# Kernel optimization log

Hardware: AMD Instinct MI355X
Metric: run time of the kernel (lower is better)

## Reference

```python
import jax, jax.numpy as jnp
import numpy as np

N_NODES, N_EDGES, HID = 30000, 480000, 128
N_GRAPHS, N_CLASSES = 128, 6
BN_EPS, ADD_SCORE = 1e-5, 0.5


def setup_inputs():
    key = jax.random.key(0)
    ks = jax.random.split(key, 12)
    g = lambda i, shape: jax.random.normal(ks[i], shape, jnp.float32) * 0.05
    return dict(
        x=jax.random.normal(ks[0], (N_NODES, HID), jnp.float32),
        edge_index=jax.random.randint(ks[1], (2, N_EDGES), 0, N_NODES, jnp.int32),
        batch=jnp.sort(jax.random.randint(ks[2], (N_NODES,), 0, N_GRAPHS, jnp.int32)),
        Wl=g(3, (6, HID, HID)), bl=jnp.zeros((6, HID), jnp.float32),
        Wr=g(4, (6, HID, HID)),
        gamma=jnp.ones((6, HID), jnp.float32), beta=jnp.zeros((6, HID), jnp.float32),
        Wlin=g(5, (3, HID, 2 * HID)), blin=jnp.zeros((3, HID), jnp.float32),
        Wp=g(6, (3, 2 * HID)), bp=jnp.zeros((3,), jnp.float32),
        Wf1=g(7, (HID, HID)), bf1=jnp.zeros((HID,), jnp.float32),
        Wf2=g(8, (N_CLASSES, HID)), bf2=jnp.zeros((N_CLASSES,), jnp.float32),
    )


def _sage(x, src, dst, emf, Wl_i, bl_i, Wr_i, N):
    # PyG SAGEConv: lin_l(mean_{j->i} x_j) + lin_r(x_i); emf masks dead edges
    msg = x[src] * emf[:, None]                              # [E,H]
    s = jax.ops.segment_sum(msg, dst, num_segments=N)
    c = jax.ops.segment_sum(emf, dst, num_segments=N)
    mean = s / jnp.maximum(c, 1.0)[:, None]
    return mean @ Wl_i.T + bl_i + x @ Wr_i.T


def _bn(x, g, b, nvf):
    # training-mode BatchNorm over valid (non-merged-away) nodes only
    cnt = jnp.maximum(nvf.sum(), 1.0)
    mu = (x * nvf[:, None]).sum(0) / cnt
    var = (((x - mu) ** 2) * nvf[:, None]).sum(0) / cnt
    return g * (x - mu) * jax.lax.rsqrt(var + BN_EPS) + b


def _edge_pool(x, src, dst, emb, nvb, Wp_i, bp_i, N, E):
    h = x.shape[1]
    # raw edge score = Linear(cat(x[src], x[dst]))
    raw = (x @ Wp_i[:h])[src] + (x @ Wp_i[h:])[dst] + bp_i   # [E]
    neg = jnp.finfo(x.dtype).min
    mx = jax.ops.segment_max(jnp.where(emb, raw, neg), dst, num_segments=N)
    z = jnp.where(emb, jnp.exp(jnp.where(emb, raw - mx[dst], 0.0)), 0.0)
    den = jax.ops.segment_sum(z, dst, num_segments=N)
    score = z / jnp.maximum(den, 1e-16)[dst] + ADD_SCORE     # softmax per dst + 0.5

    # greedy edge matching in descending score order (sequential, int-only carry)
    order = jnp.argsort(-jnp.where(emb, jax.lax.stop_gradient(score), -jnp.inf))

    def step(carry, i):
        matched, cluster, chosen = carry
        s, t = src[i], dst[i]
        ok = emb[i] & (~matched[s]) & (~matched[t]) & (s != t)
        rep, oth = jnp.minimum(s, t), jnp.maximum(s, t)
        matched = matched.at[s].set(matched[s] | ok)
        matched = matched.at[t].set(matched[t] | ok)
        cluster = cluster.at[oth].set(jnp.where(ok, rep, cluster[oth]))
        chosen = chosen.at[rep].set(jnp.where(ok, i, chosen[rep]))
        return (matched, cluster, chosen), None

    init = (~nvb, jnp.arange(N, dtype=jnp.int32), jnp.full((N,), -1, jnp.int32))
    (matched, cluster, chosen), _ = jax.lax.scan(step, init, order)

    # merged node = (x_s + x_t) * score(chosen edge); singleton score = 1
    nscore = jnp.where(chosen >= 0, score[jnp.maximum(chosen, 0)], 1.0)
    new_x = jax.ops.segment_sum(x, cluster, num_segments=N) * nscore[:, None]
    nvb2 = nvb & (cluster == jnp.arange(N, dtype=jnp.int32))
    # remap edges to cluster representatives; coalesce duplicates (self-loops kept, as PyG)
    key = jnp.where(emb, cluster[src] * N + cluster[dst], -1)  # N*N < 2**31
    uk = jnp.unique(key, size=E, fill_value=-1)
    emb2 = uk >= 0
    ukc = jnp.maximum(uk, 0)
    return new_x, ukc // N, ukc % N, emb2, nvb2


def reference(x, edge_index, batch, Wl, bl, Wr, gamma, beta, Wlin, blin, Wp, bp, Wf1, bf1, Wf2, bf2):
    N, E = x.shape[0], edge_index.shape[1]
    src, dst = edge_index[0], edge_index[1]
    emb = jnp.ones((E,), bool)   # edge-valid mask (fixed-shape graph coarsening)
    nvb = jnp.ones((N,), bool)   # node-valid mask
    for blk in range(3):
        emf, nvf = emb.astype(x.dtype), nvb.astype(x.dtype)
        i = 2 * blk
        h = _bn(jax.nn.relu(_sage(x, src, dst, emf, Wl[i], bl[i], Wr[i], N)), gamma[i], beta[i], nvf)
        h2 = _bn(jax.nn.relu(_sage(h, src, dst, emf, Wl[i + 1], bl[i + 1], Wr[i + 1], N)), gamma[i + 1], beta[i + 1], nvf)
        x = jnp.concatenate([h2, h], axis=1) @ Wlin[blk].T + blin[blk]  # dropout = identity (eval)
        x, src, dst, emb, nvb = _edge_pool(x, src, dst, emb, nvb, Wp[blk], bp[blk], N, E)
    nvf = nvb.astype(x.dtype)
    sums = jax.ops.segment_sum(x * nvf[:, None], batch, num_segments=N_GRAPHS)
    cnt = jax.ops.segment_sum(nvf, batch, num_segments=N_GRAPHS)
    pooled = sums / jnp.maximum(cnt, 1.0)[:, None]           # global_mean_pool
    hfc = jax.nn.relu(pooled @ Wf1.T + bf1)
    return jax.nn.log_softmax(hfc @ Wf2.T + bf2, axis=1)
```

## Files before the change

### kernel.cpp

```cpp
#include <hip/hip_runtime.h>
#include <stdint.h>

#define NN 30000
#define NE 480000
#define HID 128
#define NG 128
#define NC 6
#define BN_EPS 1e-5f
#define WPB 938

typedef unsigned int u32;
typedef unsigned long long u64;

__global__ void k_init(const int* __restrict__ ei, int* srcA, int* dstA, int* nvb,
                       int* scal, int* b3, int* i2, float* gbuf) {
  int t = blockIdx.x * 256 + threadIdx.x;
  if (t < NE) { srcA[t] = ei[t]; dstA[t] = ei[NE + t]; }
  if (t < NN) nvb[t] = 1;
  if (t < 2 * NN) { b3[t] = 0; i2[t] = 0; }
  if (t < NG * HID + NG) gbuf[t] = 0.f;
  if (t == 0) { scal[0] = NE; scal[1] = 0; }
}

__global__ void k_csr_count(const int* __restrict__ pE, const int* __restrict__ src,
                            const int* __restrict__ dst, int* __restrict__ cnt,
                            int* __restrict__ icnt, const int* __restrict__ nvb,
                            int* __restrict__ pcnt) {
  int t = blockIdx.x * 256 + threadIdx.x;
  if (t < NN && nvb[t]) atomicAdd(pcnt, 1);
  if (t < *pE) {
    int s = src[t], d = dst[t];
    atomicAdd(&cnt[d], 1);
    if (s != d) { atomicAdd(&icnt[s], 1); atomicAdd(&icnt[d], 1); }
  }
}

__global__ __launch_bounds__(1024) void k_scan2(const int* __restrict__ in0, int* __restrict__ out0,
                                                const int* __restrict__ in1, int* __restrict__ out1) {
  const int* in = blockIdx.x ? in1 : in0;
  int* out = blockIdx.x ? out1 : out0;
  __shared__ int part[1024];
  int t = threadIdx.x;
  int chunk = (NN + 1023) / 1024;
  int b = t * chunk, e = b + chunk;
  if (b > NN) b = NN;
  if (e > NN) e = NN;
  int s = 0;
  for (int i = b; i < e; i++) s += in[i];
  part[t] = s;
  __syncthreads();
  for (int off = 1; off < 1024; off <<= 1) {
    int v = (t >= off) ? part[t - off] : 0;
    __syncthreads();
    part[t] += v;
    __syncthreads();
  }
  int excl = (t == 0) ? 0 : part[t - 1];
  for (int i = b; i < e; i++) { out[i] = excl; excl += in[i]; }
  if (t == 0) out[NN] = part[1023];
}

__global__ void k_csr_scatter(const int* __restrict__ pE, const int* __restrict__ src,
                              const int* __restrict__ dst, const int* __restrict__ coff,
                              int* __restrict__ cursor, int* __restrict__ eids,
                              const int* __restrict__ ioff, int* __restrict__ icur,
                              int* __restrict__ ieids) {
  int e = blockIdx.x * 256 + threadIdx.x;
  if (e >= *pE) return;
  int s = src[e], d = dst[e];
  int pos = coff[d] + atomicAdd(&cursor[d], 1);
  eids[pos] = e;
  if (s != d) {
    int p1 = ioff[s] + atomicAdd(&icur[s], 1); ieids[p1] = e;
    int p2 = ioff[d] + atomicAdd(&icur[d], 1); ieids[p2] = e;
  }
}

__global__ __launch_bounds__(256) void k_sage_gather(
    const int* __restrict__ coff, const int* __restrict__ eids,
    const int* __restrict__ src, const float* __restrict__ x,
    float* __restrict__ mean) {
  int grp = threadIdx.x >> 5;
  int lane = threadIdx.x & 31;
  int n = blockIdx.x * 8 + grp;
  if (n >= NN) return;
  int b = coff[n], e2 = coff[n + 1];
  float4 acc = make_float4(0.f, 0.f, 0.f, 0.f);
  for (int i = b; i < e2; i++) {
    int s = src[eids[i]];
    float4 v = *(const float4*)(x + (size_t)s * HID + lane * 4);
    acc.x += v.x; acc.y += v.y; acc.z += v.z; acc.w += v.w;
  }
  float inv = 1.0f / fmaxf((float)(e2 - b), 1.0f);
  acc.x *= inv; acc.y *= inv; acc.z *= inv; acc.w *= inv;
  *(float4*)(mean + (size_t)n * HID + lane * 4) = acc;
}

__global__ __launch_bounds__(256) void gemm_dual(
    const float* __restrict__ A1, const float* __restrict__ W1,
    const float* __restrict__ A2, const float* __restrict__ W2,
    const float* __restrict__ bias, float* __restrict__ out,
    int M, int ldw, int relu, double* __restrict__ bnsum) {
  if (blockIdx.x == 0 && threadIdx.x < 2 * HID) bnsum[threadIdx.x] = 0.0;
  __shared__ float As[64][33];
  __shared__ float Ws[32][132];
  int row0 = blockIdx.x * 64;
  int tid = threadIdx.x;
  int cid = tid & 31;
  int rid = tid >> 5;
  float acc[8][4];
#pragma unroll
  for (int r = 0; r < 8; r++)
#pragma unroll
    for (int c = 0; c < 4; c++) acc[r][c] = 0.f;

  for (int srcI = 0; srcI < 2; ++srcI) {
    const float* A = srcI ? A2 : A1;
    const float* W = srcI ? W2 : W1;
    for (int kc = 0; kc < 128; kc += 32) {
#pragma unroll
      for (int i = 0; i < 2; ++i) {
        int idx = tid + i * 256;
        int r = idx >> 3;
        int c4 = (idx & 7) << 2;
        int gr = row0 + r;
        float4 v = make_float4(0.f, 0.f, 0.f, 0.f);
        if (gr < M) v = *(const float4*)(A + (size_t)gr * 128 + kc + c4);
        As[r][c4 + 0] = v.x; As[r][c4 + 1] = v.y; As[r][c4 + 2] = v.z; As[r][c4 + 3] = v.w;
      }
#pragma unroll
      for (int i = 0; i < 4; ++i) {
        int idx = tid + i * 256;
        int j = idx >> 3;
        int c4 = (idx & 7) << 2;
        float4 v = *(const float4*)(W + (size_t)j * ldw + kc + c4);
        Ws[c4 + 0][j] = v.x; Ws[c4 + 1][j] = v.y; Ws[c4 + 2][j] = v.z; Ws[c4 + 3][j] = v.w;
      }
      __syncthreads();
#pragma unroll
      for (int kk = 0; kk < 32; ++kk) {
        float4 w = *(const float4*)(&Ws[kk][cid * 4]);
#pragma unroll
        for (int r = 0; r < 8; ++r) {
          float a = As[rid * 8 + r][kk];
          acc[r][0] += a * w.x; acc[r][1] += a * w.y; acc[r][2] += a * w.z; acc[r][3] += a * w.w;
        }
      }
      __syncthreads();
    }
  }
#pragma unroll
  for (int r = 0; r < 8; ++r) {
    int gr = row0 + rid * 8 + r;
    if (gr >= M) continue;
#pragma unroll
    for (int c = 0; c < 4; ++c) {
      float v = acc[r][c] + bias[cid * 4 + c];
      if (relu) v = fmaxf(v, 0.f);
      out[(size_t)gr * 128 + cid * 4 + c] = v;
    }
  }
}

__global__ __launch_bounds__(128) void k_bn_stats(const float* __restrict__ x,
                                                  const int* __restrict__ nvb,
                                                  double* __restrict__ sums) {
  int k = threadIdx.x;
  int n0 = blockIdx.x * 64;
  float s = 0.f, q = 0.f;
  for (int r = 0; r < 64; r++) {
    int n = n0 + r;
    if (n >= NN) break;
    if (!nvb[n]) continue;
    float v = x[(size_t)n * HID + k];
    s += v; q += v * v;
  }
  atomicAdd(&sums[k], (double)s);
  atomicAdd(&sums[HID + k], (double)q);
}

__global__ void k_bn_apply(float* __restrict__ x, const double* __restrict__ sums,
                           const int* __restrict__ cnt, const float* __restrict__ gamma,
                           const float* __restrict__ beta) {
  int t = blockIdx.x * 256 + threadIdx.x;
  if (t >= NN * HID) return;
  int k = t & 127;
  double c = (double)((*cnt > 1) ? *cnt : 1);
  double mu = sums[k] / c;
  double var = sums[HID + k] / c - mu * mu;
  if (var < 0.0) var = 0.0;
  float inv = (float)(1.0 / sqrt(var + (double)BN_EPS));
  x[t] = gamma[k] * (x[t] - (float)mu) * inv + beta[k];
}

__global__ void k_node_proj(const float* __restrict__ x, const float* __restrict__ Wp,
                            float* __restrict__ px1, float* __restrict__ px2) {
  int n = blockIdx.x * 256 + threadIdx.x;
  if (n >= NN) return;
  const float* xr = x + (size_t)n * HID;
  float s1 = 0.f, s2 = 0.f;
#pragma unroll 8
  for (int k = 0; k < HID; k += 4) {
    float4 v = *(const float4*)(xr + k);
    float4 w1 = *(const float4*)(Wp + k);
    float4 w2 = *(const float4*)(Wp + HID + k);
    s1 += v.x * w1.x + v.y * w1.y + v.z * w1.z + v.w * w1.w;
    s2 += v.x * w2.x + v.y * w2.y + v.z * w2.z + v.w * w2.w;
  }
  px1[n] = s1; px2[n] = s2;
}

__global__ void k_edge_softmax_seed(
    const int* __restrict__ coff, const int* __restrict__ eids,
    const int* __restrict__ src, const float* __restrict__ px1,
    const float* __restrict__ px2, const float* __restrict__ bp,
    float* __restrict__ score, u64* __restrict__ ekey,
    int* __restrict__ cluster, int* __restrict__ chosen, u64* __restrict__ S) {
  int n = blockIdx.x * 256 + threadIdx.x;
  if (n >= NN) return;
  cluster[n] = n;
  chosen[n] = -1;
  S[n] = 0ull;
  int b = coff[n], e2 = coff[n + 1];
  if (b == e2) return;
  float p2 = px2[n] + *bp;
  float mx = -3.4e38f;
  for (int i = b; i < e2; i++) {
    float r = px1[src[eids[i]]] + p2;
    mx = fmaxf(mx, r);
  }
  double den = 0.0;
  for (int i = b; i < e2; i++) {
    int eid = eids[i];
    float z = expf(px1[src[eid]] + p2 - mx);
    score[eid] = z;
    den += (double)z;
  }
  if (den < 1e-16) den = 1e-16;
  double invd = 1.0 / den;
  for (int i = b; i < e2; i++) {
    int eid = eids[i];
    float sc = (float)((double)score[eid] * invd) + 0.5f;
    score[eid] = sc;
    ekey[eid] = ((u64)__float_as_uint(sc) << 32) | (u64)(0xFFFFFFFFu - (u32)eid);
  }
}

__global__ __launch_bounds__(256) void k_suitor(
    const int* __restrict__ ioff, const int* __restrict__ ieids,
    const int* __restrict__ src, const int* __restrict__ dst,
    const u64* __restrict__ ekey, u64* __restrict__ S) {
  int wid = threadIdx.x >> 6;
  int lane = threadIdx.x & 63;
  int n = blockIdx.x * 4 + wid;
  if (n >= NN) return;
  int cur = n;
  while (cur >= 0) {
    int b = ioff[cur], e2 = ioff[cur + 1];
    u64 bestKey = 0;
    for (int i = b + lane; i < e2; i += 64) {
      int e = ieids[i];
      u64 k = ekey[e];
      if (k <= bestKey) continue;
      int s = src[e], d = dst[e];
      int v = (s == cur) ? d : s;
      u64 sv = __hip_atomic_load(&S[v], __ATOMIC_RELAXED, __HIP_MEMORY_SCOPE_AGENT);
      if (k > sv) bestKey = k;
    }
#pragma unroll
    for (int o = 32; o > 0; o >>= 1) {
      u64 other = __shfl_xor(bestKey, o, 64);
      if (other > bestKey) bestKey = other;
    }
    int next = -1;
    if (bestKey != 0) {
      if (lane == 0) {
        int e = (int)(0xFFFFFFFFu - (u32)(bestKey & 0xFFFFFFFFull));
        int s = src[e], d = dst[e];
        int bestV = (s == cur) ? d : s;
        u64 old = atomicMax(&S[bestV], bestKey);
        if (old >= bestKey) {
          next = cur;
        } else if (old != 0) {
          int eo = (int)(0xFFFFFFFFu - (u32)(old & 0xFFFFFFFFull));
          int so = src[eo], do_ = dst[eo];
          next = (so == bestV) ? do_ : so;
        }
      }
      next = __shfl(next, 0, 64);
    }
    cur = next;
  }
}

__global__ void k_resolve(const int* __restrict__ src, const int* __restrict__ dst,
                          const u64* __restrict__ S, int* __restrict__ cluster,
                          int* __restrict__ chosen) {
  int n = blockIdx.x * 256 + threadIdx.x;
  if (n >= NN) return;
  u64 k = S[n];
  if (!k) return;
  int e = (int)(0xFFFFFFFFu - (u32)(k & 0xFFFFFFFFull));
  int s = src[e], d = dst[e];
  int rep = s < d ? s : d;
  if (n != rep) return;
  if (S[s] == k && S[d] == k) {
    int oth = s < d ? d : s;
    cluster[oth] = rep;
    chosen[rep] = e;
  }
}

__global__ __launch_bounds__(256) void k_new_x(
    const int* __restrict__ cluster, const int* __restrict__ chosen,
    const int* __restrict__ src, const int* __restrict__ dst,
    const float* __restrict__ score, const float* __restrict__ x,
    float* __restrict__ out, int* __restrict__ nvb, int* __restrict__ b3zero) {
  int gt = blockIdx.x * 256 + threadIdx.x;
  if (gt < 2 * NN) b3zero[gt] = 0;
  int grp = threadIdx.x >> 5;
  int lane = threadIdx.x & 31;
  int n = blockIdx.x * 8 + grp;
  if (n >= NN) return;
  float4 v = make_float4(0.f, 0.f, 0.f, 0.f);
  bool rep = (cluster[n] == n);
  if (rep) {
    v = *(const float4*)(x + (size_t)n * HID + lane * 4);
    int ch = chosen[n];
    if (ch >= 0) {
      int s = src[ch], d = dst[ch];
      int partner = (s == n) ? d : s;
      float4 w = *(const float4*)(x + (size_t)partner * HID + lane * 4);
      float sc = score[ch];
      v.x = (v.x + w.x) * sc; v.y = (v.y + w.y) * sc;
      v.z = (v.z + w.z) * sc; v.w = (v.w + w.w) * sc;
    }
  }
  *(float4*)(out + (size_t)n * HID + lane * 4) = v;
  if (lane == 0) nvb[n] = (nvb[n] && rep) ? 1 : 0;
}

__global__ void k_bucket_count(const int* __restrict__ pE, const int* __restrict__ src,
                               const int* __restrict__ cluster, int* __restrict__ bcount) {
  int e = blockIdx.x * 256 + threadIdx.x;
  if (e >= *pE) return;
  atomicAdd(&bcount[cluster[src[e]]], 1);
}

__global__ __launch_bounds__(1024) void k_scan(const int* __restrict__ in, int* __restrict__ out,
                                               int n, int* totalDst) {
  __shared__ int part[1024];
  int t = threadIdx.x;
  int chunk = (n + 1023) / 1024;
  int b = t * chunk, e = b + chunk;
  if (b > n) b = n;
  if (e > n) e = n;
  int s = 0;
  for (int i = b; i < e; i++) s += in[i];
  part[t] = s;
  __syncthreads();
  for (int off = 1; off < 1024; off <<= 1) {
    int v = (t >= off) ? part[t - off] : 0;
    __syncthreads();
    part[t] += v;
    __syncthreads();
  }
  int excl = (t == 0) ? 0 : part[t - 1];
  int total = part[1023];
  for (int i = b; i < e; i++) { out[i] = excl; excl += in[i]; }
  if (t == 0) {
    out[n] = total;
    if (totalDst) *totalDst = total;
  }
}

__global__ void k_bucket_scatter(const int* __restrict__ pE, const int* __restrict__ src,
                                 const int* __restrict__ dst, const int* __restrict__ cluster,
                                 const int* __restrict__ boffs, int* __restrict__ bcursor,
                                 int* __restrict__ bucket) {
  int e = blockIdx.x * 256 + threadIdx.x;
  if (e >= *pE) return;
  int cs = cluster[src[e]], cd = cluster[dst[e]];
  int pos = boffs[cs] + atomicAdd(&bcursor[cs], 1);
  bucket[pos] = cd;
}

__global__ __launch_bounds__(256) void k_dedup_bitmap(
    const int* __restrict__ boffs, int* __restrict__ bucket,
    int* __restrict__ ucount) {
  __shared__ u32 bm[4][960];
  int wid = threadIdx.x >> 6;
  int lane = threadIdx.x & 63;
  int n = blockIdx.x * 4 + wid;
  int b = boffs[n], e = boffs[n + 1];
  for (int w = lane; w < 960; w += 64) bm[wid][w] = 0;
  __syncthreads();
  for (int i = b + lane; i < e; i += 64)
    atomicOr(&bm[wid][bucket[i] >> 5], 1u << (bucket[i] & 31));
  __syncthreads();
  int w0 = lane * 15;
  int w1 = w0 + 15; if (w1 > WPB) w1 = WPB;
  int cnt = 0;
  for (int w = w0; w < w1; w++) cnt += __popc(bm[wid][w]);
  int inc = cnt;
  for (int o = 1; o < 64; o <<= 1) { int v = __shfl_up(inc, o); if (lane >= o) inc += v; }
  int excl = inc - cnt;
  int total = __shfl(inc, 63);
  int pos = b + excl;
  for (int w = w0; w < w1; w++) {
    u32 v = bm[wid][w];
    while (v) { int bit = __ffs(v) - 1; bucket[pos++] = (w << 5) | bit; v &= v - 1; }
  }
  if (lane == 0) ucount[n] = total;
}

__global__ void k_emit(const int* __restrict__ boffs, const int* __restrict__ bucket,
                       const int* __restrict__ bucount, const int* __restrict__ bnoffs,
                       int* __restrict__ srcO, int* __restrict__ dstO,
                       int* __restrict__ b3zero, int* __restrict__ i2zero,
                       int* __restrict__ pcnt) {
  int t = blockIdx.x * 256 + threadIdx.x;
  int stride = gridDim.x * 256;
  for (int z = t; z < 2 * NN; z += stride) { b3zero[z] = 0; i2zero[z] = 0; }
  if (t == 0) *pcnt = 0;
  if (t >= NN) return;
  int u = bucount[t], b = boffs[t], o = bnoffs[t];
  for (int i = 0; i < u; i++) { srcO[o + i] = t; dstO[o + i] = bucket[b + i]; }
}

__global__ void k_graph_pool(const int* __restrict__ nvb, const int* __restrict__ batch,
                             const float* __restrict__ x, float* __restrict__ gsum,
                             float* __restrict__ gcnt) {
  int t = blockIdx.x * 256 + threadIdx.x;
  int n = t >> 2;
  if (n >= NN) return;
  if (!nvb[n]) return;
  int sub = t & 3;
  int g = batch[n];
  const float* xr = x + (size_t)n * HID + sub * 32;
  float* o = gsum + (size_t)g * HID + sub * 32;
#pragma unroll
  for (int i = 0; i < 8; i++) {
    float4 v = *(const float4*)(xr + i * 4);
    atomicAdd(o + i * 4 + 0, v.x); atomicAdd(o + i * 4 + 1, v.y);
    atomicAdd(o + i * 4 + 2, v.z); atomicAdd(o + i * 4 + 3, v.w);
  }
  if (sub == 0) atomicAdd(&gcnt[g], 1.0f);
}

__global__ __launch_bounds__(128) void k_head1(const float* __restrict__ gsum,
                                               const float* __restrict__ gcnt,
                                               const float* __restrict__ Wf1,
                                               const float* __restrict__ bf1,
                                               float* __restrict__ hfc) {
  int g = blockIdx.x;
  int j = threadIdx.x;
  __shared__ float p[HID];
  float c = fmaxf(gcnt[g], 1.f);
  p[j] = gsum[g * HID + j] / c;
  __syncthreads();
  float s = bf1[j];
  const float* w = Wf1 + (size_t)j * HID;
  for (int k = 0; k < HID; k++) s += p[k] * w[k];
  hfc[g * HID + j] = fmaxf(s, 0.f);
}

__global__ void k_head2(const float* __restrict__ hfc, const float* __restrict__ Wf2,
                        const float* __restrict__ bf2, float* __restrict__ out) {
  int g = blockIdx.x;
  int t = threadIdx.x;
  __shared__ float lg[NC];
  if (t < NC) {
    float s = bf2[t];
    const float* w = Wf2 + (size_t)t * HID;
    const float* h = hfc + (size_t)g * HID;
    for (int k = 0; k < HID; k++) s += h[k] * w[k];
    lg[t] = s;
  }
  __syncthreads();
  if (t == 0) {
    float m = lg[0];
    for (int c = 1; c < NC; c++) m = fmaxf(m, lg[c]);
    float se = 0.f;
    for (int c = 0; c < NC; c++) se += expf(lg[c] - m);
    float lse = m + logf(se);
    for (int c = 0; c < NC; c++) out[g * NC + c] = lg[c] - lse;
  }
}

extern "C" void kernel_launch(void* const* d_in, const int* in_sizes, int n_in,
                              void* d_out, int out_size, void* d_ws, size_t ws_size,
                              hipStream_t stream) {
  const float* x0 = (const float*)d_in[0];
  const int* ei = (const int*)d_in[1];
  const int* batch = (const int*)d_in[2];
  const float* Wl = (const float*)d_in[3];
  const float* bl = (const float*)d_in[4];
  const float* Wr = (const float*)d_in[5];
  const float* gamma = (const float*)d_in[6];
  const float* beta = (const float*)d_in[7];
  const float* Wlin = (const float*)d_in[8];
  const float* blin = (const float*)d_in[9];
  const float* Wp = (const float*)d_in[10];
  const float* bp = (const float*)d_in[11];
  const float* Wf1 = (const float*)d_in[12];
  const float* bf1 = (const float*)d_in[13];
  const float* Wf2 = (const float*)d_in[14];
  const float* bf2 = (const float*)d_in[15];
  float* out = (float*)d_out;

  const int NH = NN * HID;
  size_t off = 0;
  char* base = (char*)d_ws;
  auto carve = [&](size_t bytes) -> char* {
    char* p = base + off;
    off += (bytes + 255) & ~(size_t)255;
    return p;
  };
  float* xa = (float*)carve((size_t)NH * 4);
  float* xb = (float*)carve((size_t)NH * 4);
  float* xc = (float*)carve((size_t)NH * 4);
  float* xd = (float*)carve((size_t)NH * 4);
  int* srcA = (int*)carve((size_t)NE * 4);
  int* dstA = (int*)carve((size_t)NE * 4);
  int* srcB = (int*)carve((size_t)NE * 4);
  int* dstB = (int*)carve((size_t)NE * 4);
  float* escore = (float*)carve((size_t)NE * 4);
  int* ebucket = (int*)carve((size_t)NE * 4);
  int* eids = (int*)carve((size_t)NE * 4);
  u64* ekey = (u64*)carve((size_t)NE * 8);
  int* ieids = (int*)carve((size_t)2 * NE * 4);
  u64* S = (u64*)carve((size_t)NN * 8);
  float* npx1 = (float*)carve((size_t)NN * 4);
  float* npx2 = (float*)carve((size_t)NN * 4);
  int* ncluster = (int*)carve((size_t)NN * 4);
  int* nchosen = (int*)carve((size_t)NN * 4);
  int* nvb = (int*)carve((size_t)NN * 4);
  int* b3 = (int*)carve((size_t)3 * NN * 4);
  int* bcount = b3;
  int* bcursor = b3 + NN;
  int* bucount = b3 + 2 * NN;
  int* i2 = (int*)carve((size_t)2 * NN * 4);
  int* icnt = i2;
  int* icursor = i2 + NN;
  int* boffs = (int*)carve((size_t)(NN + 1) * 4);
  int* bnoffs = (int*)carve((size_t)(NN + 1) * 4);
  int* csroff = (int*)carve((size_t)(NN + 1) * 4);
  int* ioff = (int*)carve((size_t)(NN + 1) * 4);
  double* bnsum = (double*)carve((size_t)2 * HID * 8);
  float* gbuf = (float*)carve((size_t)(NG * HID + NG) * 4);
  float* gsum = gbuf;
  float* gcnt = gbuf + NG * HID;
  float* ghfc = (float*)carve((size_t)NG * HID * 4);
  int* scal = (int*)carve(64 * 4);
  (void)ws_size; (void)n_in; (void)in_sizes; (void)out_size;

  int* pE = scal;
  int* pcnt = scal + 1;

  hipMemcpyAsync(xa, x0, (size_t)NH * 4, hipMemcpyDeviceToDevice, stream);
  k_init<<<1875, 256, 0, stream>>>(ei, srcA, dstA, nvb, scal, b3, i2, gbuf);

  int* srcC = srcA; int* dstC = dstA; int* srcN = srcB; int* dstN = dstB;
  float* xcur = xa;
  float* xtmp = xd;

  auto sage = [&](const float* xin, float* xout, int L) {
    k_sage_gather<<<3750, 256, 0, stream>>>(csroff, eids, srcC, xin, xtmp);
    gemm_dual<<<469, 256, 0, stream>>>(xtmp, Wl + (size_t)L * HID * HID, xin,
                                       Wr + (size_t)L * HID * HID, bl + (size_t)L * HID,
                                       xout, NN, HID, 1, bnsum);
    k_bn_stats<<<469, 128, 0, stream>>>(xout, nvb, bnsum);
    k_bn_apply<<<15000, 256, 0, stream>>>(xout, bnsum, pcnt, gamma + (size_t)L * HID,
                                          beta + (size_t)L * HID);
  };

  for (int b = 0; b < 3; b++) {
    k_csr_count<<<1875, 256, 0, stream>>>(pE, srcC, dstC, bcount, icnt, nvb, pcnt);
    k_scan2<<<2, 1024, 0, stream>>>(bcount, csroff, icnt, ioff);
    k_csr_scatter<<<1875, 256, 0, stream>>>(pE, srcC, dstC, csroff, bcursor, eids,
                                            ioff, icursor, ieids);

    sage(xcur, xb, 2 * b);
    sage(xb, xc, 2 * b + 1);
    gemm_dual<<<469, 256, 0, stream>>>(xc, Wlin + (size_t)b * HID * 2 * HID, xb,
                                       Wlin + (size_t)b * HID * 2 * HID + HID,
                                       blin + (size_t)b * HID, xcur, NN, 2 * HID, 0, bnsum);

    k_node_proj<<<118, 256, 0, stream>>>(xcur, Wp + (size_t)b * 2 * HID, npx1, npx2);
    k_edge_softmax_seed<<<118, 256, 0, stream>>>(csroff, eids, srcC, npx1, npx2, bp + b,
                                                 escore, ekey, ncluster, nchosen, S);
    k_suitor<<<7500, 256, 0, stream>>>(ioff, ieids, srcC, dstC, ekey, S);
    k_resolve<<<118, 256, 0, stream>>>(srcC, dstC, S, ncluster, nchosen);
    k_new_x<<<3750, 256, 0, stream>>>(ncluster, nchosen, srcC, dstC, escore, xcur, xtmp,
                                      nvb, b3);

    if (b < 2) {
      k_bucket_count<<<1875, 256, 0, stream>>>(pE, srcC, ncluster, bcount);
      k_scan<<<1, 1024, 0, stream>>>(bcount, boffs, NN, (int*)nullptr);
      k_bucket_scatter<<<1875, 256, 0, stream>>>(pE, srcC, dstC, ncluster, boffs, bcursor,
                                                 ebucket);
      k_dedup_bitmap<<<7500, 256, 0, stream>>>(boffs, ebucket, bucount);
      k_scan<<<1, 1024, 0, stream>>>(bucount, bnoffs, NN, pE);
      k_emit<<<235, 256, 0, stream>>>(boffs, ebucket, bucount, bnoffs, srcN, dstN,
                                      b3, i2, pcnt);
      { int* t = srcC; srcC = srcN; srcN = t; t = dstC; dstC = dstN; dstN = t; }
    }
    { float* t = xcur; xcur = xtmp; xtmp = t; }
  }

  k_graph_pool<<<469, 256, 0, stream>>>(nvb, batch, xcur, gsum, gcnt);
  k_head1<<<NG, 128, 0, stream>>>(gsum, gcnt, Wf1, bf1, ghfc);
  k_head2<<<NG, 32, 0, stream>>>(ghfc, Wf2, bf2, out);
}
```

Before: 3.108 ms.

## Cache suitor candidate edges in registers and fold resolve into new_x

In the suitor matching kernel, vertices with degree up to 256 now load their candidate keys and neighbours into per-lane register slots once. On a lost atomicMax the wave retries from those cached candidates, pruning the ones that are already dominated, instead of rescanning the whole adjacency list. The separate resolve kernel is removed. k_new_x now derives the mutual match and the cluster assignment directly from S, which saves a launch and the cluster/chosen initialisation. The risk is extra register pressure and more complex control flow in the suitor kernel.

```diff
diff --git a/kernel.cpp b/kernel.cpp
--- a/kernel.cpp
+++ b/kernel.cpp
@@ -8,6 +8,7 @@
 #define NC 6
 #define BN_EPS 1e-5f
 #define WPB 938
+#define SLOTS 4
 
 typedef unsigned int u32;
 typedef unsigned long long u64;
@@ -214,12 +215,9 @@
     const int* __restrict__ coff, const int* __restrict__ eids,
     const int* __restrict__ src, const float* __restrict__ px1,
     const float* __restrict__ px2, const float* __restrict__ bp,
-    float* __restrict__ score, u64* __restrict__ ekey,
-    int* __restrict__ cluster, int* __restrict__ chosen, u64* __restrict__ S) {
+    float* __restrict__ score, u64* __restrict__ ekey, u64* __restrict__ S) {
   int n = blockIdx.x * 256 + threadIdx.x;
   if (n >= NN) return;
-  cluster[n] = n;
-  chosen[n] = -1;
   S[n] = 0ull;
   int b = coff[n], e2 = coff[n + 1];
   if (b == e2) return;
@@ -257,87 +255,137 @@
   int cur = n;
   while (cur >= 0) {
     int b = ioff[cur], e2 = ioff[cur + 1];
-    u64 bestKey = 0;
-    for (int i = b + lane; i < e2; i += 64) {
-      int e = ieids[i];
-      u64 k = ekey[e];
-      if (k <= bestKey) continue;
-      int s = src[e], d = dst[e];
-      int v = (s == cur) ? d : s;
-      u64 sv = __hip_atomic_load(&S[v], __ATOMIC_RELAXED, __HIP_MEMORY_SCOPE_AGENT);
-      if (k > sv) bestKey = k;
-    }
-#pragma unroll
-    for (int o = 32; o > 0; o >>= 1) {
-      u64 other = __shfl_xor(bestKey, o, 64);
-      if (other > bestKey) bestKey = other;
-    }
-    int next = -1;
-    if (bestKey != 0) {
-      if (lane == 0) {
+    int deg = e2 - b;
+    if (deg == 0) break;
+    if (deg <= 64 * SLOTS) {
+      u64 key[SLOTS]; int pv[SLOTS];
+#pragma unroll
+      for (int s = 0; s < SLOTS; s++) {
+        key[s] = 0; pv[s] = 0;
+        int i = b + s * 64 + lane;
+        if (i < e2) {
+          int e = ieids[i];
+          key[s] = ekey[e];
+          int es = src[e], ed = dst[e];
+          pv[s] = (es == cur) ? ed : es;
+        }
+      }
+      long long res;
+      for (;;) {
+        u64 localBest = 0;
+#pragma unroll
+        for (int s = 0; s < SLOTS; s++) {
+          if (!key[s]) continue;
+          u64 sv = __hip_atomic_load(&S[pv[s]], __ATOMIC_RELAXED, __HIP_MEMORY_SCOPE_AGENT);
+          if (sv >= key[s]) key[s] = 0;
+          else if (key[s] > localBest) localBest = key[s];
+        }
+        u64 bestKey = localBest;
+#pragma unroll
+        for (int o = 32; o > 0; o >>= 1) {
+          u64 other = __shfl_xor(bestKey, o, 64);
+          if (other > bestKey) bestKey = other;
+        }
+        if (bestKey == 0) { res = -1; break; }
+        int ms = -1;
+#pragma unroll
+        for (int s = 0; s < SLOTS; s++)
+          if (ms < 0 && key[s] == bestKey) ms = s;
+        u64 ball = __ballot(ms >= 0);
+        int owner = (int)(__ffsll((long long)ball) - 1);
+        long long r0 = -3;
+        if (lane == owner) {
+          int bv = pv[ms];
+          u64 old = atomicMax(&S[bv], bestKey);
+          if (old >= bestKey) { key[ms] = 0; r0 = -2; }
+          else if (old == 0) r0 = -1;
+          else {
+            int eo = (int)(0xFFFFFFFFu - (u32)(old & 0xFFFFFFFFull));
+            int so = src[eo], do_ = dst[eo];
+            r0 = (so == bv) ? do_ : so;
+          }
+        }
+        res = __shfl(r0, owner, 64);
+        if (res != -2) break;
+      }
+      if (res < 0) break;
+      cur = (int)res;
+    } else {
+      u64 bestKey = 0;
+      for (int i = b + lane; i < e2; i += 64) {
+        int e = ieids[i];
+        u64 k = ekey[e];
+        if (k <= bestKey) continue;
+        int es = src[e], ed = dst[e];
+        int v = (es == cur) ? ed : es;
+        u64 sv = __hip_atomic_load(&S[v], __ATOMIC_RELAXED, __HIP_MEMORY_SCOPE_AGENT);
+        if (k > sv) bestKey = k;
+      }
+#pragma unroll
+      for (int o = 32; o > 0; o >>= 1) {
+        u64 other = __shfl_xor(bestKey, o, 64);
+        if (other > bestKey) bestKey = other;
+      }
+      long long r0 = -1;
+      if (bestKey != 0 && lane == 0) {
         int e = (int)(0xFFFFFFFFu - (u32)(bestKey & 0xFFFFFFFFull));
-        int s = src[e], d = dst[e];
-        int bestV = (s == cur) ? d : s;
-        u64 old = atomicMax(&S[bestV], bestKey);
-        if (old >= bestKey) {
-          next = cur;
-        } else if (old != 0) {
+        int es = src[e], ed = dst[e];
+        int bv = (es == cur) ? ed : es;
+        u64 old = atomicMax(&S[bv], bestKey);
+        if (old >= bestKey) r0 = cur;
+        else if (old != 0) {
           int eo = (int)(0xFFFFFFFFu - (u32)(old & 0xFFFFFFFFull));
           int so = src[eo], do_ = dst[eo];
-          next = (so == bestV) ? do_ : so;
+          r0 = (so == bv) ? do_ : so;
         }
       }
-      next = __shfl(next, 0, 64);
+      long long res = (bestKey != 0) ? __shfl(r0, 0, 64) : -1;
+      cur = (int)res;
     }
-    cur = next;
-  }
-}
-
-__global__ void k_resolve(const int* __restrict__ src, const int* __restrict__ dst,
-                          const u64* __restrict__ S, int* __restrict__ cluster,
-                          int* __restrict__ chosen) {
-  int n = blockIdx.x * 256 + threadIdx.x;
-  if (n >= NN) return;
-  u64 k = S[n];
-  if (!k) return;
-  int e = (int)(0xFFFFFFFFu - (u32)(k & 0xFFFFFFFFull));
-  int s = src[e], d = dst[e];
-  int rep = s < d ? s : d;
-  if (n != rep) return;
-  if (S[s] == k && S[d] == k) {
-    int oth = s < d ? d : s;
-    cluster[oth] = rep;
-    chosen[rep] = e;
   }
 }
 
 __global__ __launch_bounds__(256) void k_new_x(
-    const int* __restrict__ cluster, const int* __restrict__ chosen,
-    const int* __restrict__ src, const int* __restrict__ dst,
+    const u64* __restrict__ S, const int* __restrict__ src, const int* __restrict__ dst,
     const float* __restrict__ score, const float* __restrict__ x,
-    float* __restrict__ out, int* __restrict__ nvb, int* __restrict__ b3zero) {
+    float* __restrict__ out, int* __restrict__ cluster,
+    int* __restrict__ nvb, int* __restrict__ b3zero) {
   int gt = blockIdx.x * 256 + threadIdx.x;
   if (gt < 2 * NN) b3zero[gt] = 0;
   int grp = threadIdx.x >> 5;
   int lane = threadIdx.x & 31;
   int n = blockIdx.x * 8 + grp;
   if (n >= NN) return;
+  u64 k = S[n];
+  int partner = -1;
+  bool isOth = false;
+  float sc = 1.f;
+  if (k) {
+    int e = (int)(0xFFFFFFFFu - (u32)(k & 0xFFFFFFFFull));
+    int s = src[e], d = dst[e];
+    int other = (s == n) ? d : s;
+    if (S[other] == k) {
+      if (n > other) isOth = true;
+      else { partner = other; sc = score[e]; }
+    }
+  }
   float4 v = make_float4(0.f, 0.f, 0.f, 0.f);
-  bool rep = (cluster[n] == n);
-  if (rep) {
+  if (!isOth) {
     v = *(const float4*)(x + (size_t)n * HID + lane * 4);
-    int ch = chosen[n];
-    if (ch >= 0) {
-      int s = src[ch], d = dst[ch];
-      int partner = (s == n) ? d : s;
+    if (partner >= 0) {
       float4 w = *(const float4*)(x + (size_t)partner * HID + lane * 4);
-      float sc = score[ch];
       v.x = (v.x + w.x) * sc; v.y = (v.y + w.y) * sc;
       v.z = (v.z + w.z) * sc; v.w = (v.w + w.w) * sc;
     }
   }
   *(float4*)(out + (size_t)n * HID + lane * 4) = v;
-  if (lane == 0) nvb[n] = (nvb[n] && rep) ? 1 : 0;
+  if (lane == 0) {
+    int e2 = (int)(0xFFFFFFFFu - (u32)(k & 0xFFFFFFFFull));
+    int s2 = isOth ? src[e2] : n;
+    int d2 = isOth ? dst[e2] : n;
+    cluster[n] = isOth ? (s2 < d2 ? s2 : d2) : n;
+    nvb[n] = (nvb[n] && !isOth) ? 1 : 0;
+  }
 }
 
 __global__ void k_bucket_count(const int* __restrict__ pE, const int* __restrict__ src,
@@ -534,7 +582,6 @@
   float* npx1 = (float*)carve((size_t)NN * 4);
   float* npx2 = (float*)carve((size_t)NN * 4);
   int* ncluster = (int*)carve((size_t)NN * 4);
-  int* nchosen = (int*)carve((size_t)NN * 4);
   int* nvb = (int*)carve((size_t)NN * 4);
   int* b3 = (int*)carve((size_t)3 * NN * 4);
   int* bcount = b3;
@@ -589,11 +636,10 @@
 
     k_node_proj<<<118, 256, 0, stream>>>(xcur, Wp + (size_t)b * 2 * HID, npx1, npx2);
     k_edge_softmax_seed<<<118, 256, 0, stream>>>(csroff, eids, srcC, npx1, npx2, bp + b,
-                                                 escore, ekey, ncluster, nchosen, S);
+                                                 escore, ekey, S);
     k_suitor<<<7500, 256, 0, stream>>>(ioff, ieids, srcC, dstC, ekey, S);
-    k_resolve<<<118, 256, 0, stream>>>(srcC, dstC, S, ncluster, nchosen);
-    k_new_x<<<3750, 256, 0, stream>>>(ncluster, nchosen, srcC, dstC, escore, xcur, xtmp,
-                                      nvb, b3);
+    k_new_x<<<3750, 256, 0, stream>>>(S, srcC, dstC, escore, xcur, xtmp,
+                                      ncluster, nvb, b3);
 
     if (b < 2) {
       k_bucket_count<<<1875, 256, 0, stream>>>(pE, srcC, ncluster, bcount);
```

After: 3.008 ms. 3.2% less time.
